# Kernel optimization log

Hardware: AMD Instinct MI355X
Metric: run time of the kernel (lower is better)

Reference implementation:

```python
import jax, jax.numpy as jnp
import numpy as np

B = 1024      # num graphs
NPG = 128     # nodes per graph
N = B * NPG
EPG = 512     # edges per graph
E = B * EPG
D = 64
MAX_STEPS = 4
S = MAX_STEPS + 1   # max_steps + stop-step offset
T = 1.0
TB = 1.0
NEG = -1e30
STOP = -1


def setup_inputs() -> dict:
    key = jax.random.key(0)
    ks = jax.random.split(key, 24)
    edge_batch = jnp.repeat(jnp.arange(B, dtype=jnp.int32), EPG)
    src = jax.random.randint(ks[0], (E,), 0, NPG, dtype=jnp.int32) + edge_batch * NPG
    dst = jax.random.randint(ks[1], (E,), 0, NPG, dtype=jnp.int32) + edge_batch * NPG
    edge_index = jnp.stack([src, dst])
    sc = 1.0 / np.sqrt(D)
    p = lambda k, shape: (jax.random.normal(k, shape, jnp.float32) * sc)
    return dict(
        node_tokens=p(ks[2], (N, D)), edge_emb=p(ks[3], (E, D)),
        Wf1=p(ks[4], (D, D)), Wnf=p(ks[5], (D, D)), Wf2=p(ks[6], (D, D)),
        bf=jnp.zeros((D,), jnp.float32), wf=p(ks[7], (D,)),
        Wb1=p(ks[8], (D, D)), Wnb=p(ks[9], (D, D)), Wb2=p(ks[10], (D, D)),
        bb=jnp.zeros((D,), jnp.float32), wb=p(ks[11], (D,)),
        w_stop=p(ks[12], (D,)), b_stop=jnp.zeros((), jnp.float32),
        Ws=p(ks[13], (D, D)), Wu=p(ks[14], (D, D)), bu=jnp.zeros((D,), jnp.float32),
        edge_index=edge_index, edge_batch=edge_batch,
    )


def reference(node_tokens, edge_emb, Wf1, Wnf, Wf2, bf, wf,
              Wb1, Wnb, Wb2, bb, wb, w_stop, b_stop, Ws, Wu, bu,
              edge_index, edge_batch):
    esrc, edst = edge_index[0], edge_index[1]
    # state-independent part of the edge scores (precomputed once; faithful math)
    base_f = edge_emb @ Wf1 + node_tokens[esrc] @ Wnf + bf   # [E,D]
    base_b = edge_emb @ Wb1 + node_tokens[edst] @ Wnb + bb   # [E,D]
    g_ids = jnp.arange(B, dtype=jnp.int32)
    eidx = jnp.arange(E, dtype=jnp.int32)

    def seg_lse(x, valid):
        # per-graph logsumexp over valid edges (grad-safe masking)
        xm = jnp.where(valid, x, NEG)
        m = jax.ops.segment_max(xm, edge_batch, num_segments=B)
        xc = jnp.where(valid, x - m[edge_batch], 0.0)
        s = jax.ops.segment_sum(jnp.where(valid, jnp.exp(xc), 0.0), edge_batch, num_segments=B)
        return m + jnp.log(jnp.maximum(s, 1e-30))

    def step_fn(carry, k):
        state_vec, active, used, done, steps, stopn = carry
        valid = (esrc == active[edge_batch]) & (~used) & (~done[edge_batch])
        allow_stop = (~done) & (steps < MAX_STEPS)
        # forward edge scores + stop logit
        h = jax.nn.relu(base_f + (state_vec @ Wf2)[edge_batch])   # [E,D]
        score = h @ wf                                            # [E]
        stop_logit = state_vec @ w_stop + b_stop                  # [B]
        x = score / T
        lse_e = seg_lse(x, valid)
        stop_t = jnp.where(allow_stop, stop_logit / T, NEG)
        Z = jnp.logaddexp(lse_e, stop_t)
        logp_edge = x - Z[edge_batch]
        logp_stop = jnp.where(allow_stop, stop_logit / T - Z, 0.0)
        has_edge = jax.ops.segment_sum(valid.astype(jnp.int32), edge_batch, num_segments=B) > 0
        # gumbel-max sampling with scatter_max semantics
        ke, ksn = jax.random.split(k)
        se = jnp.where(valid, logp_edge + jax.random.gumbel(ke, (E,)), NEG)
        ss = jnp.where(allow_stop, logp_stop + jax.random.gumbel(ksn, (B,)), NEG)
        m = jax.ops.segment_max(se, edge_batch, num_segments=B)
        amax = jax.ops.segment_min(jnp.where(se == m[edge_batch], eidx, E), edge_batch, num_segments=B)
        amax = jnp.where(has_edge, amax, 0).astype(jnp.int32)
        m = jnp.where(has_edge, m, NEG)
        choose_stop = (ss > m) | (~has_edge)
        actions = jnp.where(choose_stop | done, STOP, amax)
        log_pf = jnp.where(choose_stop, logp_stop, logp_edge[amax])
        log_pf = jnp.where(done, 0.0, log_pf)
        take_edge = (actions >= 0) & (~done)
        stopping = choose_stop & (~done)
        stopn = jnp.where((stopn < 0) & stopping, active - g_ids * NPG, stopn)
        # state encoder update (masked)
        rel = edge_emb[amax]                                      # [B,D]
        new_state = jnp.tanh(state_vec @ Ws + rel @ Wu + bu)
        state_vec = jnp.where(take_edge[:, None], new_state, state_vec)
        # env step
        new_active = jnp.where(take_edge, edst[amax], active)
        used = used.at[amax].max(take_edge)
        steps = steps + take_edge.astype(jnp.int32)
        new_done = done | stopping
        # backward policy log-prob over edges incoming to the new active node
        bvalid = edst == new_active[edge_batch]
        hb = jax.nn.relu(base_b + (state_vec @ Wb2)[edge_batch])
        xb = (hb @ wb) / TB
        lse_b = seg_lse(xb, bvalid)
        log_pb = jnp.where(take_edge, xb[amax] - lse_b, 0.0)
        return (state_vec, new_active, used, new_done, steps, stopn), (actions, log_pf, log_pb)

    init = (
        jnp.zeros((B, D), jnp.float32),      # state_vec
        g_ids * NPG,                          # active node (global) = graph start node
        jnp.zeros((E,), bool),                # used_edge_mask
        jnp.zeros((B,), bool),                # done
        jnp.zeros((B,), jnp.int32),           # step_counts
        jnp.full((B,), STOP, jnp.int32),      # stop_node_locals
    )
    keys = jax.random.split(jax.random.key(42), S)
    (state_vec, active, used, done, steps, stopn), ys = jax.lax.scan(step_fn, init, keys)
    actions_seq = ys[0].T      # [B,S]
    log_pf_steps = ys[1].T     # [B,S]
    log_pb_steps = ys[2].T     # [B,S]
    stopn = jnp.where(stopn < 0, active - g_ids * NPG, stopn)   # backfill stop nodes
    return (actions_seq, log_pf_steps.sum(1), log_pf_steps, log_pb_steps,
            used, stopn, steps.astype(jnp.float32))
```

## Files before the change

kernel.cpp:

```cpp
#include <hip/hip_runtime.h>
#include <hip/hip_bf16.h>
#include <cstdint>

#define NBLK 1024
#define NPG  128
#define EPG  512
#define DD   64
#define NSTEP 5
#define ETOT (NBLK*EPG)
#define NEGF (-1e30f)
#define MAXDEG 32

#define OA  0
#define OLS 5120
#define OPF 6144
#define OPB 11264
#define OU  16384
#define OSN 540672
#define OST 541696

struct KeysArg {
  uint32_t ke0[NSTEP], ke1[NSTEP];
  uint32_t ks0[NSTEP], ks1[NSTEP];
};

__host__ __device__ inline uint32_t rotl32(uint32_t x, int r){ return (x<<r)|(x>>(32-r)); }

__host__ __device__ inline void tf2x32(uint32_t k0, uint32_t k1, uint32_t& x0, uint32_t& x1){
  uint32_t k2 = k0 ^ k1 ^ 0x1BD11BDAu;
  x0 += k0; x1 += k1;
  x0+=x1; x1=rotl32(x1,13); x1^=x0;
  x0+=x1; x1=rotl32(x1,15); x1^=x0;
  x0+=x1; x1=rotl32(x1,26); x1^=x0;
  x0+=x1; x1=rotl32(x1, 6); x1^=x0;
  x0+=k1; x1+=k2+1u;
  x0+=x1; x1=rotl32(x1,17); x1^=x0;
  x0+=x1; x1=rotl32(x1,29); x1^=x0;
  x0+=x1; x1=rotl32(x1,16); x1^=x0;
  x0+=x1; x1=rotl32(x1,24); x1^=x0;
  x0+=k2; x1+=k0+2u;
  x0+=x1; x1=rotl32(x1,13); x1^=x0;
  x0+=x1; x1=rotl32(x1,15); x1^=x0;
  x0+=x1; x1=rotl32(x1,26); x1^=x0;
  x0+=x1; x1=rotl32(x1, 6); x1^=x0;
  x0+=k0; x1+=k1+3u;
  x0+=x1; x1=rotl32(x1,17); x1^=x0;
  x0+=x1; x1=rotl32(x1,29); x1^=x0;
  x0+=x1; x1=rotl32(x1,16); x1^=x0;
  x0+=x1; x1=rotl32(x1,24); x1^=x0;
  x0+=k1; x1+=k2+4u;
  x0+=x1; x1=rotl32(x1,13); x1^=x0;
  x0+=x1; x1=rotl32(x1,15); x1^=x0;
  x0+=x1; x1=rotl32(x1,26); x1^=x0;
  x0+=x1; x1=rotl32(x1, 6); x1^=x0;
  x0+=k2; x1+=k0+5u;
}

__device__ inline float gumbel_from_bits(uint32_t bits){
  float f = __uint_as_float((bits>>9) | 0x3f800000u) - 1.0f;
  const float tiny = 1.17549435e-38f;
  float u = fmaxf(tiny, f * (1.0f - tiny) + tiny);
  return -logf(-logf(u));
}

__device__ inline float gumbel_part(uint32_t k0, uint32_t k1, uint32_t idx){
  uint32_t x0 = 0u, x1 = idx;
  tf2x32(k0, k1, x0, x1);
  return gumbel_from_bits(x0 ^ x1);
}

__device__ inline float wsum(float x){
  #pragma unroll
  for (int off = 32; off; off >>= 1) x += __shfl_xor(x, off, 64);
  return x;
}

__device__ __forceinline__ float rdlane(float v, int i){
  return __int_as_float(__builtin_amdgcn_readlane(__float_as_int(v), i));
}

__device__ __forceinline__ float matvec_col(const float* __restrict__ W, float v, int lane){
  float a0=0.f, a1=0.f, a2=0.f, a3=0.f;
  #pragma unroll 4
  for (int i = 0; i < DD; i += 4){
    a0 = fmaf(rdlane(v, i  ), W[(i  )*DD+lane], a0);
    a1 = fmaf(rdlane(v, i+1), W[(i+1)*DD+lane], a1);
    a2 = fmaf(rdlane(v, i+2), W[(i+2)*DD+lane], a2);
    a3 = fmaf(rdlane(v, i+3), W[(i+3)*DD+lane], a3);
  }
  return (a0+a1)+(a2+a3);
}

__device__ __forceinline__ void matvec_col2(const float* __restrict__ Wa, float va,
                                            const float* __restrict__ Wb, float vb,
                                            int lane, float& oa, float& ob){
  float a0=0.f,a1=0.f,a2=0.f,a3=0.f, b0=0.f,b1=0.f,b2=0.f,b3=0.f;
  #pragma unroll 4
  for (int i = 0; i < DD; i += 4){
    a0 = fmaf(rdlane(va, i  ), Wa[(i  )*DD+lane], a0);
    b0 = fmaf(rdlane(vb, i  ), Wb[(i  )*DD+lane], b0);
    a1 = fmaf(rdlane(va, i+1), Wa[(i+1)*DD+lane], a1);
    b1 = fmaf(rdlane(vb, i+1), Wb[(i+1)*DD+lane], b1);
    a2 = fmaf(rdlane(va, i+2), Wa[(i+2)*DD+lane], a2);
    b2 = fmaf(rdlane(vb, i+2), Wb[(i+2)*DD+lane], b2);
    a3 = fmaf(rdlane(va, i+3), Wa[(i+3)*DD+lane], a3);
    b3 = fmaf(rdlane(vb, i+3), Wb[(i+3)*DD+lane], b3);
  }
  oa = (a0+a1)+(a2+a3);
  ob = (b0+b1)+(b2+b3);
}

__device__ __forceinline__ void matvec4(const float* __restrict__ W,
                                        float v0, float v1, float v2, float v3,
                                        int lane, float o[4]){
  float acc[4][4] = {{0,0,0,0},{0,0,0,0},{0,0,0,0},{0,0,0,0}};
  #pragma unroll 4
  for (int i = 0; i < DD; i += 4){
    #pragma unroll
    for (int t = 0; t < 4; t++){
      float w  = W[(i+t)*DD+lane];
      acc[0][t] = fmaf(rdlane(v0, i+t), w, acc[0][t]);
      acc[1][t] = fmaf(rdlane(v1, i+t), w, acc[1][t]);
      acc[2][t] = fmaf(rdlane(v2, i+t), w, acc[2][t]);
      acc[3][t] = fmaf(rdlane(v3, i+t), w, acc[3][t]);
    }
  }
  #pragma unroll
  for (int c = 0; c < 4; c++)
    o[c] = (acc[c][0]+acc[c][1])+(acc[c][2]+acc[c][3]);
}

__global__ void __launch_bounds__(64)
gfn_fused(const float* __restrict__ node_tokens,
          const float* __restrict__ edge_emb,
          const float* __restrict__ Wf1, const float* __restrict__ Wnf, const float* __restrict__ Wf2,
          const float* __restrict__ bf,  const float* __restrict__ wf,
          const float* __restrict__ Wb1, const float* __restrict__ Wnb, const float* __restrict__ Wb2,
          const float* __restrict__ bb,  const float* __restrict__ wb,
          const float* __restrict__ w_stop, const float* __restrict__ b_stop,
          const float* __restrict__ Ws,  const float* __restrict__ Wu, const float* __restrict__ bu,
          const int* __restrict__ e_src, const int* __restrict__ e_dst,
          float* __restrict__ out, KeysArg keys)
{
  const int g    = blockIdx.x;
  const int lane = threadIdx.x;
  const int ebase = g * EPG;

  __shared__ uint8_t  srcL[EPG], dstL[EPG];
  __shared__ uint16_t listO[EPG], listI[EPG];
  __shared__ int cntO[NPG], cntI[NPG], begO[NPG], begI[NPG];
  __shared__ uint8_t usedL[EPG];
  __shared__ float xc[MAXDEG], gm[MAXDEG];

  #pragma unroll
  for (int r = 0; r < 8; r++){
    int j = r*64 + lane;
    srcL[j] = (uint8_t)(e_src[ebase+j] - g*NPG);
    dstL[j] = (uint8_t)(e_dst[ebase+j] - g*NPG);
    usedL[j] = 0;
  }
  cntO[lane]=0; cntO[lane+64]=0; cntI[lane]=0; cntI[lane+64]=0;

  #pragma unroll
  for (int r = 0; r < 8; r++){
    int j = r*64 + lane;
    atomicAdd(&cntO[srcL[j]], 1);
    atomicAdd(&cntI[dstL[j]], 1);
  }

  {
    int n0 = lane*2, n1 = n0+1;
    int c0O=cntO[n0], c1O=cntO[n1], sO=c0O+c1O;
    int c0I=cntI[n0], c1I=cntI[n1], sI=c0I+c1I;
    int xO=sO, xI=sI;
    #pragma unroll
    for (int off=1; off<64; off<<=1){
      int tO=__shfl_up(xO,off,64), tI=__shfl_up(xI,off,64);
      if (lane>=off){ xO+=tO; xI+=tI; }
    }
    begO[n0]=xO-sO; begO[n1]=xO-c1O;
    begI[n0]=xI-sI; begI[n1]=xI-c1I;
  }
  cntO[lane]=0; cntO[lane+64]=0; cntI[lane]=0; cntI[lane+64]=0;

  #pragma unroll
  for (int r = 0; r < 8; r++){
    int j = r*64 + lane;
    int sL = srcL[j]; int p = atomicAdd(&cntO[sL],1); listO[begO[sL]+p] = (uint16_t)j;
    int dL = dstL[j]; int q = atomicAdd(&cntI[dL],1); listI[begI[dL]+q] = (uint16_t)j;
  }

  const float bf_l = bf[lane], wf_l = wf[lane];
  const float bb_l = bb[lane], wb_l = wb[lane];
  const float bu_l = bu[lane], wst_l = w_stop[lane];
  const float bstop = b_stop[0];

  float st_v = 0.f;
  bool done = false;
  int stepsC = 0;
  int stopn = -1;
  int activeL = 0;
  float lpf_sum = 0.f;

  for (int s = 0; s < NSTEP; s++){
    float act_out = -1.f, lpf_out = 0.f, lpb_out = 0.f;
    if (!done){
      const int bO = begO[activeL];
      const int dOc = min(cntO[activeL], MAXDEG);

      float ntv = node_tokens[(size_t)(g*NPG + activeL)*DD + lane];
      float u_j, nt_j;
      matvec_col2(Wf2, st_v, Wnf, ntv, lane, u_j, nt_j);
      float sl = wsum(st_v * wst_l) + bstop;

      if (lane < dOc){
        int el = listO[bO + lane];
        gm[lane] = gumbel_part(keys.ke0[s], keys.ke1[s], (uint32_t)(ebase+el));
      }
      float gs = gumbel_part(keys.ks0[s], keys.ks1[s], (uint32_t)g);

      for (int base = 0; base < dOc; base += 4){
        int el[4]; float v[4];
        #pragma unroll
        for (int t = 0; t < 4; t++){
          int k = base + t;
          el[t] = listO[bO + min(k, dOc-1)];
          v[t]  = edge_emb[(size_t)(ebase+el[t])*DD + lane];
        }
        float o[4];
        matvec4(Wf1, v[0], v[1], v[2], v[3], lane, o);
        #pragma unroll
        for (int t = 0; t < 4; t++){
          int k = base + t;
          if (k < dOc){
            float x = NEGF;
            if (!usedL[el[t]]){
              float h = fmaxf(o[t] + nt_j + bf_l + u_j, 0.f);
              x = wsum(h * wf_l);
            }
            if (lane == 0) xc[k] = x;
          }
        }
      }

      float m1 = NEGF; int nvalid = 0;
      for (int k=0;k<dOc;k++){ float xk=xc[k]; if (xk!=NEGF){ m1=fmaxf(m1,xk); nvalid++; } }
      float ssum = 0.f;
      for (int k=0;k<dOc;k++){ float xk=xc[k]; if (xk!=NEGF) ssum += expf(xk - m1); }
      const bool has_edge = nvalid > 0;
      float lse_e = m1 + logf(fmaxf(ssum, 1e-30f));
      const bool allow_stop = (stepsC < 4);
      float stop_t = allow_stop ? sl : NEGF;
      float amx = fmaxf(lse_e, stop_t);
      float Z = amx + log1pf(expf(-fabsf(lse_e - stop_t)));

      float mbest = NEGF; int elbest = -1; float xbest = 0.f;
      for (int k=0;k<dOc;k++){
        float xk = xc[k];
        if (xk == NEGF) continue;
        float se = (xk - Z) + gm[k];
        if (se > mbest){ mbest = se; elbest = listO[bO+k]; xbest = xk; }
      }
      float ss = allow_stop ? (sl - Z) + gs : NEGF;
      float mcmp = has_edge ? mbest : NEGF;
      const bool choose_stop = (ss > mcmp) || (!has_edge);
      float logp_stop = allow_stop ? (sl - Z) : 0.f;
      const bool take_edge = !choose_stop;

      act_out = choose_stop ? -1.f : (float)(ebase + elbest);
      lpf_out = choose_stop ? logp_stop : (xbest - Z);
      if (choose_stop && stopn < 0) stopn = activeL;

      if (take_edge){
        float rv = edge_emb[(size_t)(ebase+elbest)*DD + lane];
        float acs, acr;
        matvec_col2(Ws, st_v, Wu, rv, lane, acs, acr);
        st_v = tanhf(acs + acr + bu_l);
        if (lane == 0) usedL[elbest] = 1;
        activeL = dstL[elbest];
        stepsC++;

        float nbv = node_tokens[(size_t)(g*NPG + activeL)*DD + lane];
        float ntb_j, ub_j;
        matvec_col2(Wnb, nbv, Wb2, st_v, lane, ntb_j, ub_j);

        const int bI = begI[activeL];
        const int dIc = min(cntI[activeL], MAXDEG);
        float xbb = 0.f;
        for (int base = 0; base < dIc; base += 4){
          int el[4]; float v[4];
          #pragma unroll
          for (int t = 0; t < 4; t++){
            int k = base + t;
            el[t] = listI[bI + min(k, dIc-1)];
            v[t]  = edge_emb[(size_t)(ebase+el[t])*DD + lane];
          }
          float o[4];
          matvec4(Wb1, v[0], v[1], v[2], v[3], lane, o);
          #pragma unroll
          for (int t = 0; t < 4; t++){
            int k = base + t;
            if (k < dIc){
              float h = fmaxf(o[t] + ntb_j + bb_l + ub_j, 0.f);
              float xb = wsum(h * wb_l);
              if (lane == 0) xc[k] = xb;
              if (el[t] == elbest) xbb = xb;
            }
          }
        }
        float m2 = NEGF;
        for (int k=0;k<dIc;k++) m2 = fmaxf(m2, xc[k]);
        float s2 = 0.f;
        for (int k=0;k<dIc;k++) s2 += expf(xc[k] - m2);
        float lse_b = m2 + logf(fmaxf(s2, 1e-30f));
        lpb_out = xbb - lse_b;
      }
      done = done || choose_stop;
    }

    if (lane == 0){
      out[OA  + g*NSTEP + s] = act_out;
      out[OPF + g*NSTEP + s] = lpf_out;
      out[OPB + g*NSTEP + s] = lpb_out;
    }
    lpf_sum += lpf_out;
  }

  if (lane == 0){
    out[OLS + g] = lpf_sum;
    int sn = (stopn < 0) ? activeL : stopn;
    out[OSN + g] = (float)sn;
    out[OST + g] = (float)stepsC;
  }
  #pragma unroll
  for (int r = 0; r < 8; r++){
    int j = r*64 + lane;
    out[OU + ebase + j] = usedL[j] ? 1.0f : 0.0f;
  }
}

extern "C" void kernel_launch(void* const* d_in, const int* in_sizes, int n_in,
                              void* d_out, int out_size, void* d_ws, size_t ws_size,
                              hipStream_t stream)
{
  (void)in_sizes; (void)n_in; (void)out_size; (void)d_ws; (void)ws_size;

  KeysArg K;
  for (uint32_t s = 0; s < NSTEP; s++){
    uint32_t a = 0u, b = s;
    tf2x32(0u, 42u, a, b);
    uint32_t e0 = 0u, e1 = 0u;
    tf2x32(a, b, e0, e1);
    uint32_t s0 = 0u, s1 = 1u;
    tf2x32(a, b, s0, s1);
    K.ke0[s] = e0; K.ke1[s] = e1;
    K.ks0[s] = s0; K.ks1[s] = s1;
  }

  const int* eidx = (const int*)d_in[17];
  gfn_fused<<<dim3(NBLK), dim3(64), 0, stream>>>(
      (const float*)d_in[0],  (const float*)d_in[1],
      (const float*)d_in[2],  (const float*)d_in[3],  (const float*)d_in[4],
      (const float*)d_in[5],  (const float*)d_in[6],
      (const float*)d_in[7],  (const float*)d_in[8],  (const float*)d_in[9],
      (const float*)d_in[10], (const float*)d_in[11],
      (const float*)d_in[12], (const float*)d_in[13],
      (const float*)d_in[14], (const float*)d_in[15], (const float*)d_in[16],
      eidx, eidx + ETOT,
      (float*)d_out, K);
}
```

Before: 96.53 us.

## Fuse next-step forward scoring into backward pass and batch wave reductions

Once an edge is taken, the forward edge scoring for the next step (state matvecs, gumbel noise, per-edge Wf1 matvec) now runs in the same loop as the backward scoring for the current step. The two matvec streams are interleaved through a combined 4x2 matvec and a 4-way matvec_col4. Per-edge wave reductions are batched four at a time, and the matvec4 unroll factor goes from 4 to 8. The goal is to raise ILP in a latency-bound single-wave-per-graph kernel, at the cost of more registers and more complex control flow.

```diff
diff --git a/kernel.cpp b/kernel.cpp
--- a/kernel.cpp
+++ b/kernel.cpp
@@ -75,6 +75,16 @@
   return x;
 }
 
+__device__ __forceinline__ void wsum4(float& x0, float& x1, float& x2, float& x3){
+  #pragma unroll
+  for (int off = 32; off; off >>= 1){
+    x0 += __shfl_xor(x0, off, 64);
+    x1 += __shfl_xor(x1, off, 64);
+    x2 += __shfl_xor(x2, off, 64);
+    x3 += __shfl_xor(x3, off, 64);
+  }
+}
+
 __device__ __forceinline__ float rdlane(float v, int i){
   return __int_as_float(__builtin_amdgcn_readlane(__float_as_int(v), i));
 }
@@ -110,11 +120,32 @@
   ob = (b0+b1)+(b2+b3);
 }
 
+__device__ __forceinline__ void matvec_col4(
+    const float* __restrict__ W0, float v0, const float* __restrict__ W1, float v1,
+    const float* __restrict__ W2, float v2, const float* __restrict__ W3, float v3,
+    int lane, float& o0, float& o1, float& o2, float& o3){
+  float a[4][4] = {{0,0,0,0},{0,0,0,0},{0,0,0,0},{0,0,0,0}};
+  #pragma unroll 4
+  for (int i = 0; i < DD; i += 4){
+    #pragma unroll
+    for (int t = 0; t < 4; t++){
+      a[0][t] = fmaf(rdlane(v0, i+t), W0[(i+t)*DD+lane], a[0][t]);
+      a[1][t] = fmaf(rdlane(v1, i+t), W1[(i+t)*DD+lane], a[1][t]);
+      a[2][t] = fmaf(rdlane(v2, i+t), W2[(i+t)*DD+lane], a[2][t]);
+      a[3][t] = fmaf(rdlane(v3, i+t), W3[(i+t)*DD+lane], a[3][t]);
+    }
+  }
+  o0 = (a[0][0]+a[0][1])+(a[0][2]+a[0][3]);
+  o1 = (a[1][0]+a[1][1])+(a[1][2]+a[1][3]);
+  o2 = (a[2][0]+a[2][1])+(a[2][2]+a[2][3]);
+  o3 = (a[3][0]+a[3][1])+(a[3][2]+a[3][3]);
+}
+
 __device__ __forceinline__ void matvec4(const float* __restrict__ W,
                                         float v0, float v1, float v2, float v3,
                                         int lane, float o[4]){
   float acc[4][4] = {{0,0,0,0},{0,0,0,0},{0,0,0,0},{0,0,0,0}};
-  #pragma unroll 4
+  #pragma unroll 8
   for (int i = 0; i < DD; i += 4){
     #pragma unroll
     for (int t = 0; t < 4; t++){
@@ -128,6 +159,34 @@
   #pragma unroll
   for (int c = 0; c < 4; c++)
     o[c] = (acc[c][0]+acc[c][1])+(acc[c][2]+acc[c][3]);
+}
+
+__device__ __forceinline__ void matvec4x2(const float* __restrict__ Wa, const float va[4],
+                                          const float* __restrict__ Wb, const float vb[4],
+                                          int lane, float oa[4], float ob[4]){
+  float A[4][4] = {{0,0,0,0},{0,0,0,0},{0,0,0,0},{0,0,0,0}};
+  float B[4][4] = {{0,0,0,0},{0,0,0,0},{0,0,0,0},{0,0,0,0}};
+  #pragma unroll 8
+  for (int i = 0; i < DD; i += 4){
+    #pragma unroll
+    for (int t = 0; t < 4; t++){
+      float wa = Wa[(i+t)*DD+lane];
+      float wb = Wb[(i+t)*DD+lane];
+      A[0][t] = fmaf(rdlane(va[0], i+t), wa, A[0][t]);
+      B[0][t] = fmaf(rdlane(vb[0], i+t), wb, B[0][t]);
+      A[1][t] = fmaf(rdlane(va[1], i+t), wa, A[1][t]);
+      B[1][t] = fmaf(rdlane(vb[1], i+t), wb, B[1][t]);
+      A[2][t] = fmaf(rdlane(va[2], i+t), wa, A[2][t]);
+      B[2][t] = fmaf(rdlane(vb[2], i+t), wb, B[2][t]);
+      A[3][t] = fmaf(rdlane(va[3], i+t), wa, A[3][t]);
+      B[3][t] = fmaf(rdlane(vb[3], i+t), wb, B[3][t]);
+    }
+  }
+  #pragma unroll
+  for (int c = 0; c < 4; c++){
+    oa[c] = (A[c][0]+A[c][1])+(A[c][2]+A[c][3]);
+    ob[c] = (B[c][0]+B[c][1])+(B[c][2]+B[c][3]);
+  }
 }
 
 __global__ void __launch_bounds__(64)
@@ -150,7 +209,8 @@
   __shared__ uint16_t listO[EPG], listI[EPG];
   __shared__ int cntO[NPG], cntI[NPG], begO[NPG], begI[NPG];
   __shared__ uint8_t usedL[EPG];
-  __shared__ float xc[MAXDEG], gm[MAXDEG];
+  __shared__ float xcF[MAXDEG], gmF[MAXDEG];
+  __shared__ float xcB[MAXDEG];
 
   #pragma unroll
   for (int r = 0; r < 8; r++){
@@ -197,74 +257,65 @@
 
   float st_v = 0.f;
   bool done = false;
-  int stepsC = 0;
-  int stopn = -1;
-  int activeL = 0;
+  int stepsC = 0, stopn = -1, activeL = 0;
   float lpf_sum = 0.f;
+
+  int bOF, dOF; float slF, gsF;
+  {
+    float ntv = node_tokens[(size_t)(g*NPG + activeL)*DD + lane];
+    float u_j, nt_j;
+    matvec_col2(Wf2, st_v, Wnf, ntv, lane, u_j, nt_j);
+    slF = wsum(st_v * wst_l) + bstop;
+    bOF = begO[activeL]; dOF = min(cntO[activeL], MAXDEG);
+    if (lane < dOF)
+      gmF[lane] = gumbel_part(keys.ke0[0], keys.ke1[0], (uint32_t)(ebase + listO[bOF+lane]));
+    gsF = gumbel_part(keys.ks0[0], keys.ks1[0], (uint32_t)g);
+    for (int base = 0; base < dOF; base += 4){
+      int el[4]; float v[4];
+      #pragma unroll
+      for (int t = 0; t < 4; t++){
+        int k = base + t;
+        el[t] = listO[bOF + min(k, dOF-1)];
+        v[t]  = edge_emb[(size_t)(ebase+el[t])*DD + lane];
+      }
+      float o[4], x[4];
+      matvec4(Wf1, v[0], v[1], v[2], v[3], lane, o);
+      #pragma unroll
+      for (int t = 0; t < 4; t++) x[t] = fmaxf(o[t] + nt_j + bf_l + u_j, 0.f) * wf_l;
+      wsum4(x[0], x[1], x[2], x[3]);
+      #pragma unroll
+      for (int t = 0; t < 4; t++){
+        int k = base + t;
+        if (k < dOF && lane == 0) xcF[k] = usedL[el[t]] ? NEGF : x[t];
+      }
+    }
+  }
 
   for (int s = 0; s < NSTEP; s++){
     float act_out = -1.f, lpf_out = 0.f, lpb_out = 0.f;
     if (!done){
-      const int bO = begO[activeL];
-      const int dOc = min(cntO[activeL], MAXDEG);
-
-      float ntv = node_tokens[(size_t)(g*NPG + activeL)*DD + lane];
-      float u_j, nt_j;
-      matvec_col2(Wf2, st_v, Wnf, ntv, lane, u_j, nt_j);
-      float sl = wsum(st_v * wst_l) + bstop;
-
-      if (lane < dOc){
-        int el = listO[bO + lane];
-        gm[lane] = gumbel_part(keys.ke0[s], keys.ke1[s], (uint32_t)(ebase+el));
-      }
-      float gs = gumbel_part(keys.ks0[s], keys.ks1[s], (uint32_t)g);
-
-      for (int base = 0; base < dOc; base += 4){
-        int el[4]; float v[4];
-        #pragma unroll
-        for (int t = 0; t < 4; t++){
-          int k = base + t;
-          el[t] = listO[bO + min(k, dOc-1)];
-          v[t]  = edge_emb[(size_t)(ebase+el[t])*DD + lane];
-        }
-        float o[4];
-        matvec4(Wf1, v[0], v[1], v[2], v[3], lane, o);
-        #pragma unroll
-        for (int t = 0; t < 4; t++){
-          int k = base + t;
-          if (k < dOc){
-            float x = NEGF;
-            if (!usedL[el[t]]){
-              float h = fmaxf(o[t] + nt_j + bf_l + u_j, 0.f);
-              x = wsum(h * wf_l);
-            }
-            if (lane == 0) xc[k] = x;
-          }
-        }
-      }
-
       float m1 = NEGF; int nvalid = 0;
-      for (int k=0;k<dOc;k++){ float xk=xc[k]; if (xk!=NEGF){ m1=fmaxf(m1,xk); nvalid++; } }
+      for (int k=0;k<dOF;k++){ float xk=xcF[k]; if (xk!=NEGF){ m1=fmaxf(m1,xk); nvalid++; } }
       float ssum = 0.f;
-      for (int k=0;k<dOc;k++){ float xk=xc[k]; if (xk!=NEGF) ssum += expf(xk - m1); }
+      for (int k=0;k<dOF;k++){ float xk=xcF[k]; if (xk!=NEGF) ssum += expf(xk - m1); }
       const bool has_edge = nvalid > 0;
       float lse_e = m1 + logf(fmaxf(ssum, 1e-30f));
       const bool allow_stop = (stepsC < 4);
-      float stop_t = allow_stop ? sl : NEGF;
+      float stop_t = allow_stop ? slF : NEGF;
       float amx = fmaxf(lse_e, stop_t);
       float Z = amx + log1pf(expf(-fabsf(lse_e - stop_t)));
 
       float mbest = NEGF; int elbest = -1; float xbest = 0.f;
-      for (int k=0;k<dOc;k++){
-        float xk = xc[k];
+      for (int k=0;k<dOF;k++){
+        float xk = xcF[k];
         if (xk == NEGF) continue;
-        float se = (xk - Z) + gm[k];
-        if (se > mbest){ mbest = se; elbest = listO[bO+k]; xbest = xk; }
+        float se = (xk - Z) + gmF[k];
+        if (se > mbest){ mbest = se; elbest = listO[bOF+k]; xbest = xk; }
       }
-      float ss = allow_stop ? (sl - Z) + gs : NEGF;
+      float ss = allow_stop ? (slF - Z) + gsF : NEGF;
       float mcmp = has_edge ? mbest : NEGF;
       const bool choose_stop = (ss > mcmp) || (!has_edge);
-      float logp_stop = allow_stop ? (sl - Z) : 0.f;
+      float logp_stop = allow_stop ? (slF - Z) : 0.f;
       const bool take_edge = !choose_stop;
 
       act_out = choose_stop ? -1.f : (float)(ebase + elbest);
@@ -281,39 +332,85 @@
         stepsC++;
 
         float nbv = node_tokens[(size_t)(g*NPG + activeL)*DD + lane];
-        float ntb_j, ub_j;
-        matvec_col2(Wnb, nbv, Wb2, st_v, lane, ntb_j, ub_j);
-
-        const int bI = begI[activeL];
-        const int dIc = min(cntI[activeL], MAXDEG);
+        const int bI = begI[activeL], dIc = min(cntI[activeL], MAXDEG);
+        float ntb_j, ub_j, uN = 0.f, ntN = 0.f;
+        int bON = 0, dON = 0;
+        if (s < NSTEP-1){
+          matvec_col4(Wnb, nbv, Wb2, st_v, Wf2, st_v, Wnf, nbv,
+                      lane, ntb_j, ub_j, uN, ntN);
+          bON = begO[activeL]; dON = min(cntO[activeL], MAXDEG);
+          slF = wsum(st_v * wst_l) + bstop;
+          if (lane < dON)
+            gmF[lane] = gumbel_part(keys.ke0[s+1], keys.ke1[s+1],
+                                    (uint32_t)(ebase + listO[bON+lane]));
+          gsF = gumbel_part(keys.ks0[s+1], keys.ks1[s+1], (uint32_t)g);
+        } else {
+          matvec_col2(Wnb, nbv, Wb2, st_v, lane, ntb_j, ub_j);
+        }
+
         float xbb = 0.f;
-        for (int base = 0; base < dIc; base += 4){
-          int el[4]; float v[4];
-          #pragma unroll
-          for (int t = 0; t < 4; t++){
-            int k = base + t;
-            el[t] = listI[bI + min(k, dIc-1)];
-            v[t]  = edge_emb[(size_t)(ebase+el[t])*DD + lane];
+        const int nbch = (dIc + 3) >> 2;
+        const int nfch = (s < NSTEP-1) ? ((dON + 3) >> 2) : 0;
+        const int nch = max(nbch, nfch);
+        for (int c = 0; c < nch; c++){
+          const bool hasB = c < nbch, hasF = c < nfch;
+          int elB[4], elF[4]; float vB[4], vF[4];
+          float oB[4], oF[4];
+          if (hasB){
+            #pragma unroll
+            for (int t = 0; t < 4; t++){
+              int k = c*4 + t;
+              elB[t] = listI[bI + min(k, dIc-1)];
+              vB[t]  = edge_emb[(size_t)(ebase+elB[t])*DD + lane];
+            }
           }
-          float o[4];
-          matvec4(Wb1, v[0], v[1], v[2], v[3], lane, o);
-          #pragma unroll
-          for (int t = 0; t < 4; t++){
-            int k = base + t;
-            if (k < dIc){
-              float h = fmaxf(o[t] + ntb_j + bb_l + ub_j, 0.f);
-              float xb = wsum(h * wb_l);
-              if (lane == 0) xc[k] = xb;
-              if (el[t] == elbest) xbb = xb;
+          if (hasF){
+            #pragma unroll
+            for (int t = 0; t < 4; t++){
+              int k = c*4 + t;
+              elF[t] = listO[bON + min(k, dON-1)];
+              vF[t]  = edge_emb[(size_t)(ebase+elF[t])*DD + lane];
+            }
+          }
+          if (hasB && hasF)      matvec4x2(Wb1, vB, Wf1, vF, lane, oB, oF);
+          else if (hasB)         matvec4(Wb1, vB[0], vB[1], vB[2], vB[3], lane, oB);
+          else                   matvec4(Wf1, vF[0], vF[1], vF[2], vF[3], lane, oF);
+
+          if (hasB){
+            float xb[4];
+            #pragma unroll
+            for (int t = 0; t < 4; t++) xb[t] = fmaxf(oB[t] + ntb_j + bb_l + ub_j, 0.f) * wb_l;
+            wsum4(xb[0], xb[1], xb[2], xb[3]);
+            #pragma unroll
+            for (int t = 0; t < 4; t++){
+              int k = c*4 + t;
+              if (k < dIc){
+                if (lane == 0) xcB[k] = xb[t];
+                if (elB[t] == elbest) xbb = xb[t];
+              }
+            }
+          }
+          if (hasF){
+            float x[4];
+            #pragma unroll
+            for (int t = 0; t < 4; t++) x[t] = fmaxf(oF[t] + ntN + bf_l + uN, 0.f) * wf_l;
+            wsum4(x[0], x[1], x[2], x[3]);
+            #pragma unroll
+            for (int t = 0; t < 4; t++){
+              int k = c*4 + t;
+              if (k < dON && lane == 0) xcF[k] = usedL[elF[t]] ? NEGF : x[t];
             }
           }
         }
+
         float m2 = NEGF;
-        for (int k=0;k<dIc;k++) m2 = fmaxf(m2, xc[k]);
+        for (int k=0;k<dIc;k++) m2 = fmaxf(m2, xcB[k]);
         float s2 = 0.f;
-        for (int k=0;k<dIc;k++) s2 += expf(xc[k] - m2);
+        for (int k=0;k<dIc;k++) s2 += expf(xcB[k] - m2);
         float lse_b = m2 + logf(fmaxf(s2, 1e-30f));
         lpb_out = xbb - lse_b;
+
+        bOF = bON; dOF = dON;
       }
       done = done || choose_stop;
     }
```

Result: slower. 101.1 us (+4.8%).
